# Optimization experiments

Hardware: AMD Instinct MI355X
Metric: run time of the kernel (lower is better)

The kernel has to match this reference:

```python
import jax, jax.numpy as jnp
import numpy as np

N_LETTERS = 256
EMBED_DIM = 1024
HIDDEN_DIM = 2048
SEQ_LEN = 4096


def setup_inputs() -> dict:
    key = jax.random.key(0)
    ks = jax.random.split(key, 8)
    s_e = 1.0 / np.sqrt(EMBED_DIM)
    s_h = 1.0 / np.sqrt(HIDDEN_DIM)
    return {
        "input_ids": jax.random.randint(ks[0], (SEQ_LEN,), 0, N_LETTERS, dtype=jnp.int64)
        if jax.config.jax_enable_x64 else jax.random.randint(ks[0], (SEQ_LEN,), 0, N_LETTERS, dtype=jnp.int32),
        "h0": jnp.zeros((1, 1, HIDDEN_DIM), jnp.float32),
        "c0": jnp.zeros((1, 1, HIDDEN_DIM), jnp.float32),
        "W_emb": jax.random.normal(ks[1], (N_LETTERS, EMBED_DIM), jnp.float32),
        "W_ih": jax.random.normal(ks[2], (4 * HIDDEN_DIM, EMBED_DIM), jnp.float32) * s_e,
        "W_hh": jax.random.normal(ks[3], (4 * HIDDEN_DIM, HIDDEN_DIM), jnp.float32) * s_h,
        "b_ih": jnp.zeros((4 * HIDDEN_DIM,), jnp.float32),
        "b_hh": jnp.zeros((4 * HIDDEN_DIM,), jnp.float32),
        "W_out": jax.random.normal(ks[4], (N_LETTERS, HIDDEN_DIM), jnp.float32) * s_h,
        "b_out": jnp.zeros((N_LETTERS,), jnp.float32),
    }


def reference(input_ids, h0, c0, W_emb, W_ih, W_hh, b_ih, b_hh, W_out, b_out):
    H = W_hh.shape[1]
    emb = W_emb[input_ids]                       # [L, E]
    # Precompute the input-side gate projections for all timesteps (batched GEMM).
    x_gates = emb @ W_ih.T + (b_ih + b_hh)       # [L, 4H]

    def step(carry, xg):
        h, c = carry                             # [H], [H]
        gates = xg + W_hh @ h                    # [4H], PyTorch order i,f,g,o
        i = jax.nn.sigmoid(gates[0 * H:1 * H])
        f = jax.nn.sigmoid(gates[1 * H:2 * H])
        g = jnp.tanh(gates[2 * H:3 * H])
        o = jax.nn.sigmoid(gates[3 * H:4 * H])
        c_new = f * c + i * g
        h_new = o * jnp.tanh(c_new)
        return (h_new, c_new), h_new

    (hL, cL), hs = jax.lax.scan(step, (h0[0, 0], c0[0, 0]), x_gates)  # hs: [L, H]
    logits = hs @ W_out.T + b_out                # [L, n_letters]
    # Dropout(p=0.1) is identity in eval mode.
    out = jax.nn.log_softmax(jax.nn.relu(logits), axis=-1)
    return out, hL[None, None, :], cL[None, None, :]
```

## Files before the change

kernel.cpp:

```cpp
#include <hip/hip_runtime.h>
#include <hip/hip_bf16.h>

#define SEQ 4096
#define EMB 1024
#define HID 2048
#define G4  8192
#define NL  256

typedef __attribute__((ext_vector_type(8))) short bf16x8;
typedef __attribute__((ext_vector_type(4))) float f32x4;

static __device__ __forceinline__ unsigned short f2bf(float f) {
    unsigned int x = __builtin_bit_cast(unsigned int, f);
    return (unsigned short)((x + 0x7FFFu + ((x >> 16) & 1u)) >> 16);
}
static __device__ __forceinline__ float bf2f(unsigned short u) {
    return __builtin_bit_cast(float, ((unsigned int)u) << 16);
}
static __device__ __forceinline__ unsigned long long aload(const unsigned long long* p) {
    return __hip_atomic_load(p, __ATOMIC_RELAXED, __HIP_MEMORY_SCOPE_AGENT);
}
static __device__ __forceinline__ float fsigm(float x) {
    return 1.f / (1.f + __expf(-x));
}
static __device__ __forceinline__ float ftanh(float x) {
    return 1.f - 2.f / (__expf(2.f * x) + 1.f);
}

__global__ __launch_bounds__(256) void k_f2b(const float* __restrict__ in,
                                             unsigned short* __restrict__ out, int n) {
    int i = (blockIdx.x * 256 + threadIdx.x) * 4;
    if (i < n) {
        float4 v = *(const float4*)&in[i];
        ushort4 u;
        u.x = f2bf(v.x); u.y = f2bf(v.y); u.z = f2bf(v.z); u.w = f2bf(v.w);
        *(ushort4*)&out[i] = u;
    }
}

__global__ __launch_bounds__(256) void k_emb(const int* __restrict__ ids,
                                             const float* __restrict__ W_emb,
                                             unsigned short* __restrict__ out) {
    int t = blockIdx.x;
    int e0 = threadIdx.x * 4;
    const float4 v = *(const float4*)&W_emb[(size_t)ids[t] * EMB + e0];
    ushort4 u;
    u.x = f2bf(v.x); u.y = f2bf(v.y); u.z = f2bf(v.z); u.w = f2bf(v.w);
    *(ushort4*)&out[(size_t)t * EMB + e0] = u;
}

#define BM 128
#define BN 128
#define BK 32
__global__ __launch_bounds__(256) void k_gemm_bt(
    const unsigned short* __restrict__ A, const unsigned short* __restrict__ B,
    const float* __restrict__ bias1, const float* __restrict__ bias2,
    float* __restrict__ Cf, unsigned short* __restrict__ Cb,
    int M, int N, int K)
{
    __shared__ unsigned short As[BM * BK];
    __shared__ unsigned short Bs[BN * BK];
    const int bm = blockIdx.x * BM;
    const int bn = blockIdx.y * BN;
    const int tid = threadIdx.x;
    const int wave = tid >> 6, lane = tid & 63;
    const int wm = (wave & 1) * 64, wn = (wave >> 1) * 64;
    const int row16 = lane & 15, quad = lane >> 4;

    f32x4 acc[4][4];
#pragma unroll
    for (int i = 0; i < 4; ++i)
#pragma unroll
        for (int j = 0; j < 4; ++j) acc[i][j] = (f32x4){0.f, 0.f, 0.f, 0.f};

    for (int k0 = 0; k0 < K; k0 += BK) {
        __syncthreads();
#pragma unroll
        for (int s = 0; s < 2; ++s) {
            int c = tid + s * 256;
            int r = c >> 2, col = (c & 3) * 8;
            *(uint4*)&As[r * BK + col] = *(const uint4*)&A[(size_t)(bm + r) * K + k0 + col];
            *(uint4*)&Bs[r * BK + col] = *(const uint4*)&B[(size_t)(bn + r) * K + k0 + col];
        }
        __syncthreads();
        bf16x8 af[4], bfr[4];
#pragma unroll
        for (int i = 0; i < 4; ++i) {
            af[i]  = *(const bf16x8*)&As[(wm + i * 16 + row16) * BK + quad * 8];
            bfr[i] = *(const bf16x8*)&Bs[(wn + i * 16 + row16) * BK + quad * 8];
        }
#pragma unroll
        for (int i = 0; i < 4; ++i)
#pragma unroll
            for (int j = 0; j < 4; ++j)
                acc[i][j] = __builtin_amdgcn_mfma_f32_16x16x32_bf16(af[i], bfr[j], acc[i][j], 0, 0, 0);
    }

#pragma unroll
    for (int j = 0; j < 4; ++j) {
        int col = bn + wn + j * 16 + row16;
        float bsum = (bias1 ? bias1[col] : 0.f) + (bias2 ? bias2[col] : 0.f);
#pragma unroll
        for (int i = 0; i < 4; ++i) {
#pragma unroll
            for (int r = 0; r < 4; ++r) {
                int row = bm + wm + i * 16 + quad * 4 + r;
                float v = acc[i][j][r] + bsum;
                if (Cf) Cf[(size_t)row * N + col] = v;
                else    Cb[(size_t)row * N + col] = f2bf(v);
            }
        }
    }
}

#define LSTM_LDS 90112
__global__ __launch_bounds__(1024, 1) void k_lstm(
    const unsigned short* __restrict__ Whhb,
    const unsigned short* __restrict__ xg,
    const float* __restrict__ h0, const float* __restrict__ c0,
    unsigned short* __restrict__ hsb,
    float* __restrict__ outHC,
    unsigned long long* __restrict__ hcomm)
{
    extern __shared__ char smem[];
    float* LDSp = (float*)smem;

    const int b = blockIdx.x, tid = threadIdx.x;
    const int wave = tid >> 6, lane = tid & 63;
    const int sub = lane & 15, quad = lane >> 4;

    const int qa = (sub >> 3), qb = 2 + (sub >> 3), j = sub & 7;
    const unsigned short* wa = Whhb + ((size_t)(qa * HID + b * 8 + j)) * HID + wave * 128 + quad * 8;
    const unsigned short* wb = Whhb + ((size_t)(qb * HID + b * 8 + j)) * HID + wave * 128 + quad * 8;
    bf16x8 afrA[4], afrB[4];
#pragma unroll
    for (int c = 0; c < 4; ++c) {
        afrA[c] = *(const bf16x8*)(wa + c * 32);
        afrB[c] = *(const bf16x8*)(wb + c * 32);
    }

    float creg = 0.f;
    if (tid < 8) creg = c0[b * 8 + tid];

    for (int t = 0; t < SEQ; ++t) {
        float xq0 = 0.f, xq1 = 0.f, xq2 = 0.f, xq3 = 0.f;
        if (wave == 0 && lane < 8) {
            const unsigned short* xr = xg + (size_t)t * G4 + b * 8 + lane;
            xq0 = bf2f(xr[0]);
            xq1 = bf2f(xr[2048]);
            xq2 = bf2f(xr[4096]);
            xq3 = bf2f(xr[6144]);
        }

        f32x4 acc0 = (f32x4){0.f, 0.f, 0.f, 0.f};
        f32x4 acc1 = (f32x4){0.f, 0.f, 0.f, 0.f};

        if (t == 0) {
#pragma unroll
            for (int c = 0; c < 4; ++c) {
                const float* hp = h0 + wave * 128 + c * 32 + quad * 8;
                float4 va = *(const float4*)hp;
                float4 vb = *(const float4*)(hp + 4);
                uint4 d;
                d.x = (unsigned)f2bf(va.x) | ((unsigned)f2bf(va.y) << 16);
                d.y = (unsigned)f2bf(va.z) | ((unsigned)f2bf(va.w) << 16);
                d.z = (unsigned)f2bf(vb.x) | ((unsigned)f2bf(vb.y) << 16);
                d.w = (unsigned)f2bf(vb.z) | ((unsigned)f2bf(vb.w) << 16);
                bf16x8 hf = __builtin_bit_cast(bf16x8, d);
                acc0 = __builtin_amdgcn_mfma_f32_16x16x32_bf16(afrA[c], hf, acc0, 0, 0, 0);
                acc1 = __builtin_amdgcn_mfma_f32_16x16x32_bf16(afrB[c], hf, acc1, 0, 0, 0);
            }
        } else {
            const unsigned long long* src =
                hcomm + (size_t)((t - 1) & 1) * 8192 + (size_t)(b & 7) * 1024 + wave * 64;
            const unsigned tag = (unsigned)t;
            unsigned long long x;
            for (;;) {
                x = aload(&src[lane]);
                if ((unsigned)(x >> 32) == tag) break;
                __builtin_amdgcn_s_sleep(1);
            }
            int myd = (int)(unsigned)x;
#pragma unroll
            for (int c = 0; c < 4; ++c) {
                const int sl = c * 16 + quad * 4;
                uint4 d;
                d.x = (unsigned)__shfl(myd, sl + 0);
                d.y = (unsigned)__shfl(myd, sl + 1);
                d.z = (unsigned)__shfl(myd, sl + 2);
                d.w = (unsigned)__shfl(myd, sl + 3);
                bf16x8 hf = __builtin_bit_cast(bf16x8, d);
                acc0 = __builtin_amdgcn_mfma_f32_16x16x32_bf16(afrA[c], hf, acc0, 0, 0, 0);
                acc1 = __builtin_amdgcn_mfma_f32_16x16x32_bf16(afrB[c], hf, acc1, 0, 0, 0);
            }
        }

        float* P = LDSp + (t & 1) * 640;
        if (sub == 0) {
#pragma unroll
            for (int r = 0; r < 4; ++r) {
                P[(quad * 4 + r) * 20 + wave]      = acc0[r];
                P[(16 + quad * 4 + r) * 20 + wave] = acc1[r];
            }
        }
        __syncthreads();

        if (wave == 0) {
            float g = 0.f;
            if (lane < 32) {
                const float* rp = P + lane * 20;
                f32x4 s = *(const f32x4*)rp;
                s += *(const f32x4*)(rp + 4);
                s += *(const f32x4*)(rp + 8);
                s += *(const f32x4*)(rp + 12);
                g = s[0] + s[1] + s[2] + s[3];
            }
            float gF = __shfl(g, 8 + lane);
            float gG = __shfl(g, 16 + lane);
            float gO = __shfl(g, 24 + lane);
            unsigned hv = 0;
            float cn = 0.f, hn = 0.f;
            if (lane < 8) {
                float gi = g  + xq0;
                float gf = gF + xq1;
                float gg = gG + xq2;
                float go = gO + xq3;
                float i_ = fsigm(gi);
                float f_ = fsigm(gf);
                float g_ = ftanh(gg);
                float o_ = fsigm(go);
                cn = f_ * creg + i_ * g_;
                hn = o_ * ftanh(cn);
                creg = cn;
                hv = (unsigned)f2bf(hn);
            }
            {
                int jj = lane & 3;
                unsigned lo = (unsigned)__shfl((int)hv, 2 * jj);
                unsigned hi = (unsigned)__shfl((int)hv, 2 * jj + 1);
                if (lane < 32) {
                    unsigned long long wrd =
                        (((unsigned long long)(unsigned)(t + 1)) << 32)
                        | (unsigned long long)(lo | (hi << 16));
                    __hip_atomic_store(
                        &hcomm[(size_t)(t & 1) * 8192 + (size_t)(lane >> 2) * 1024 + b * 4 + jj],
                        wrd, __ATOMIC_RELAXED, __HIP_MEMORY_SCOPE_AGENT);
                }
            }
            if (lane < 8) {
                hsb[(size_t)t * HID + b * 8 + lane] = (unsigned short)hv;
                if (t == SEQ - 1) {
                    outHC[b * 8 + lane] = hn;
                    outHC[HID + b * 8 + lane] = cn;
                }
            }
        }
    }
}

__global__ __launch_bounds__(256) void k_softmax(const float* __restrict__ logits,
                                                 float* __restrict__ out) {
    int row = blockIdx.x * 4 + (threadIdx.x >> 6);
    int lane = threadIdx.x & 63;
    const float* Lr = logits + (size_t)row * NL;
    float4 v = *(const float4*)&Lr[lane * 4];
    v.x = fmaxf(v.x, 0.f); v.y = fmaxf(v.y, 0.f);
    v.z = fmaxf(v.z, 0.f); v.w = fmaxf(v.w, 0.f);
    float m = fmaxf(fmaxf(v.x, v.y), fmaxf(v.z, v.w));
#pragma unroll
    for (int off = 32; off > 0; off >>= 1) m = fmaxf(m, __shfl_xor(m, off));
    float e = __expf(v.x - m) + __expf(v.y - m) + __expf(v.z - m) + __expf(v.w - m);
#pragma unroll
    for (int off = 32; off > 0; off >>= 1) e += __shfl_xor(e, off);
    float ls = __logf(e) + m;
    float4 o;
    o.x = v.x - ls; o.y = v.y - ls; o.z = v.z - ls; o.w = v.w - ls;
    *(float4*)&out[(size_t)row * NL + lane * 4] = o;
}

extern "C" void kernel_launch(void* const* d_in, const int* in_sizes, int n_in,
                              void* d_out, int out_size, void* d_ws, size_t ws_size,
                              hipStream_t stream) {
    const int*   ids   = (const int*)d_in[0];
    const float* h0    = (const float*)d_in[1];
    const float* c0    = (const float*)d_in[2];
    const float* W_emb = (const float*)d_in[3];
    const float* W_ih  = (const float*)d_in[4];
    const float* W_hh  = (const float*)d_in[5];
    const float* b_ih  = (const float*)d_in[6];
    const float* b_hh  = (const float*)d_in[7];
    const float* W_out = (const float*)d_in[8];
    const float* b_out = (const float*)d_in[9];
    float* out = (float*)d_out;

    char* ws = (char*)d_ws;
    unsigned short* xg    = (unsigned short*)(ws);
    unsigned short* hsb   = (unsigned short*)(ws + 67108864);
    unsigned short* Wihb  = (unsigned short*)(ws + 83886080);
    unsigned short* embb  = (unsigned short*)(ws + 100663296);
    unsigned short* Woutb = (unsigned short*)(ws + 109051904);
    float*          logit = (float*)(ws + 110100480);
    unsigned short* Whhb  = (unsigned short*)(ws + 114294784);
    unsigned long long* hcomm = (unsigned long long*)(ws + 147849216);

    k_f2b<<<(G4 * EMB / 4 + 255) / 256, 256, 0, stream>>>(W_ih, Wihb, G4 * EMB);
    k_f2b<<<(NL * HID / 4 + 255) / 256, 256, 0, stream>>>(W_out, Woutb, NL * HID);
    k_f2b<<<(G4 * HID / 4 + 255) / 256, 256, 0, stream>>>(W_hh, Whhb, G4 * HID);
    k_emb<<<SEQ, 256, 0, stream>>>(ids, W_emb, embb);

    dim3 g1(SEQ / BM, G4 / BN);
    k_gemm_bt<<<g1, 256, 0, stream>>>(embb, Wihb, b_ih, b_hh, nullptr, xg, SEQ, G4, EMB);

    hipFuncSetAttribute((const void*)k_lstm, hipFuncAttributeMaxDynamicSharedMemorySize, LSTM_LDS);
    k_lstm<<<256, 1024, LSTM_LDS, stream>>>(Whhb, xg, h0, c0, hsb, out + (size_t)SEQ * NL, hcomm);

    dim3 g2(SEQ / BM, NL / BN);
    k_gemm_bt<<<g2, 256, 0, stream>>>(hsb, Woutb, b_out, nullptr, logit, nullptr, SEQ, NL, HID);

    k_softmax<<<SEQ / 4, 256, 0, stream>>>(logit, out);
}
```

Baseline: 10.61 ms.

## Interleave x_gates layout, split MFMA chains, tune polling and prioritize gate wave

The GEMM that produces bf16 x_gates now writes them gate-interleaved, so each hidden unit's four gate values sit next to each other. The LSTM step can then fetch them with one 8-byte load instead of four strided loads. The MFMA accumulation is split into two independent chains per gate half to shorten the dependency chain. Polling for the previous hidden state first checks immediately, then sleeps longer between retries to reduce memory traffic. The wave on the critical gate-compute and broadcast path is given raised scheduling priority.

```diff
diff --git a/kernel.cpp b/kernel.cpp
--- a/kernel.cpp
+++ b/kernel.cpp
@@ -107,7 +107,7 @@
                 int row = bm + wm + i * 16 + quad * 4 + r;
                 float v = acc[i][j][r] + bsum;
                 if (Cf) Cf[(size_t)row * N + col] = v;
-                else    Cb[(size_t)row * N + col] = f2bf(v);
+                else    Cb[(size_t)row * N + ((col & 2047) << 2) + (col >> 11)] = f2bf(v);
             }
         }
     }
@@ -145,15 +145,17 @@
     for (int t = 0; t < SEQ; ++t) {
         float xq0 = 0.f, xq1 = 0.f, xq2 = 0.f, xq3 = 0.f;
         if (wave == 0 && lane < 8) {
-            const unsigned short* xr = xg + (size_t)t * G4 + b * 8 + lane;
-            xq0 = bf2f(xr[0]);
-            xq1 = bf2f(xr[2048]);
-            xq2 = bf2f(xr[4096]);
-            xq3 = bf2f(xr[6144]);
-        }
-
-        f32x4 acc0 = (f32x4){0.f, 0.f, 0.f, 0.f};
-        f32x4 acc1 = (f32x4){0.f, 0.f, 0.f, 0.f};
+            uint2 w2 = *(const uint2*)(xg + (size_t)t * G4 + (size_t)(b * 8 + lane) * 4);
+            xq0 = bf2f((unsigned short)(w2.x & 0xffff));
+            xq1 = bf2f((unsigned short)(w2.x >> 16));
+            xq2 = bf2f((unsigned short)(w2.y & 0xffff));
+            xq3 = bf2f((unsigned short)(w2.y >> 16));
+        }
+
+        f32x4 accA0 = (f32x4){0.f, 0.f, 0.f, 0.f};
+        f32x4 accA1 = (f32x4){0.f, 0.f, 0.f, 0.f};
+        f32x4 accB0 = (f32x4){0.f, 0.f, 0.f, 0.f};
+        f32x4 accB1 = (f32x4){0.f, 0.f, 0.f, 0.f};
 
         if (t == 0) {
 #pragma unroll
@@ -167,18 +169,26 @@
                 d.z = (unsigned)f2bf(vb.x) | ((unsigned)f2bf(vb.y) << 16);
                 d.w = (unsigned)f2bf(vb.z) | ((unsigned)f2bf(vb.w) << 16);
                 bf16x8 hf = __builtin_bit_cast(bf16x8, d);
-                acc0 = __builtin_amdgcn_mfma_f32_16x16x32_bf16(afrA[c], hf, acc0, 0, 0, 0);
-                acc1 = __builtin_amdgcn_mfma_f32_16x16x32_bf16(afrB[c], hf, acc1, 0, 0, 0);
+                if (c < 2) {
+                    accA0 = __builtin_amdgcn_mfma_f32_16x16x32_bf16(afrA[c], hf, accA0, 0, 0, 0);
+                    accB0 = __builtin_amdgcn_mfma_f32_16x16x32_bf16(afrB[c], hf, accB0, 0, 0, 0);
+                } else {
+                    accA1 = __builtin_amdgcn_mfma_f32_16x16x32_bf16(afrA[c], hf, accA1, 0, 0, 0);
+                    accB1 = __builtin_amdgcn_mfma_f32_16x16x32_bf16(afrB[c], hf, accB1, 0, 0, 0);
+                }
             }
         } else {
             const unsigned long long* src =
                 hcomm + (size_t)((t - 1) & 1) * 8192 + (size_t)(b & 7) * 1024 + wave * 64;
             const unsigned tag = (unsigned)t;
-            unsigned long long x;
-            for (;;) {
-                x = aload(&src[lane]);
-                if ((unsigned)(x >> 32) == tag) break;
-                __builtin_amdgcn_s_sleep(1);
+            unsigned long long x = aload(&src[lane]);
+            if ((unsigned)(x >> 32) != tag) {
+                __builtin_amdgcn_s_sleep(8);
+                for (;;) {
+                    x = aload(&src[lane]);
+                    if ((unsigned)(x >> 32) == tag) break;
+                    __builtin_amdgcn_s_sleep(2);
+                }
             }
             int myd = (int)(unsigned)x;
 #pragma unroll
@@ -190,10 +200,17 @@
                 d.z = (unsigned)__shfl(myd, sl + 2);
                 d.w = (unsigned)__shfl(myd, sl + 3);
                 bf16x8 hf = __builtin_bit_cast(bf16x8, d);
-                acc0 = __builtin_amdgcn_mfma_f32_16x16x32_bf16(afrA[c], hf, acc0, 0, 0, 0);
-                acc1 = __builtin_amdgcn_mfma_f32_16x16x32_bf16(afrB[c], hf, acc1, 0, 0, 0);
-            }
-        }
+                if (c < 2) {
+                    accA0 = __builtin_amdgcn_mfma_f32_16x16x32_bf16(afrA[c], hf, accA0, 0, 0, 0);
+                    accB0 = __builtin_amdgcn_mfma_f32_16x16x32_bf16(afrB[c], hf, accB0, 0, 0, 0);
+                } else {
+                    accA1 = __builtin_amdgcn_mfma_f32_16x16x32_bf16(afrA[c], hf, accA1, 0, 0, 0);
+                    accB1 = __builtin_amdgcn_mfma_f32_16x16x32_bf16(afrB[c], hf, accB1, 0, 0, 0);
+                }
+            }
+        }
+        f32x4 acc0 = accA0 + accA1;
+        f32x4 acc1 = accB0 + accB1;
 
         float* P = LDSp + (t & 1) * 640;
         if (sub == 0) {
@@ -206,6 +223,7 @@
         __syncthreads();
 
         if (wave == 0) {
+            __builtin_amdgcn_s_setprio(1);
             float g = 0.f;
             if (lane < 32) {
                 const float* rp = P + lane * 20;
@@ -247,6 +265,7 @@
                         wrd, __ATOMIC_RELAXED, __HIP_MEMORY_SCOPE_AGENT);
                 }
             }
+            __builtin_amdgcn_s_setprio(0);
             if (lane < 8) {
                 hsb[(size_t)t * HID + b * 8 + lane] = (unsigned short)hv;
                 if (t == SEQ - 1) {
```

Result: faster. 10.31 ms (-2.8%).

## Halve LSTM persistent blocks, 16 units per block with interleaved gate layout

Applied to the files above, without the earlier changes.

Each persistent LSTM block now owns 16 hidden units instead of 8, so 128 blocks run instead of 256. Each wave issues four MFMAs per k-chunk covering all four gates. The input-gate GEMM output is stored gate-interleaved, so each unit's four gate preactivations load as one 8-byte read. The change also swaps the sigmoid/tanh divisions for hardware reciprocals, polls twice per spin iteration after an initial sleep, and raises wave-0 priority during the gate update. The aim is to cut the number of blocks taking part in each step's cross-block handshake and the latency of the per-step critical path, at the cost of more work per block per step.

```diff
diff --git a/kernel.cpp b/kernel.cpp
--- a/kernel.cpp
+++ b/kernel.cpp
@@ -20,11 +20,14 @@
 static __device__ __forceinline__ unsigned long long aload(const unsigned long long* p) {
     return __hip_atomic_load(p, __ATOMIC_RELAXED, __HIP_MEMORY_SCOPE_AGENT);
 }
+static __device__ __forceinline__ float frcp(float x) {
+    return __builtin_amdgcn_rcpf(x);
+}
 static __device__ __forceinline__ float fsigm(float x) {
-    return 1.f / (1.f + __expf(-x));
+    return frcp(1.f + __expf(-x));
 }
 static __device__ __forceinline__ float ftanh(float x) {
-    return 1.f - 2.f / (__expf(2.f * x) + 1.f);
+    return 1.f - 2.f * frcp(__expf(2.f * x) + 1.f);
 }
 
 __global__ __launch_bounds__(256) void k_f2b(const float* __restrict__ in,
@@ -107,12 +110,14 @@
                 int row = bm + wm + i * 16 + quad * 4 + r;
                 float v = acc[i][j][r] + bsum;
                 if (Cf) Cf[(size_t)row * N + col] = v;
-                else    Cb[(size_t)row * N + col] = f2bf(v);
-            }
-        }
-    }
-}
-
+                else    Cb[(size_t)row * N + ((col & 2047) << 2) + (col >> 11)] = f2bf(v);
+            }
+        }
+    }
+}
+
+#define NBLK 128
+#define UPB  16
 #define LSTM_LDS 90112
 __global__ __launch_bounds__(1024, 1) void k_lstm(
     const unsigned short* __restrict__ Whhb,
@@ -129,36 +134,36 @@
     const int wave = tid >> 6, lane = tid & 63;
     const int sub = lane & 15, quad = lane >> 4;
 
-    const int qa = (sub >> 3), qb = 2 + (sub >> 3), j = sub & 7;
-    const unsigned short* wa = Whhb + ((size_t)(qa * HID + b * 8 + j)) * HID + wave * 128 + quad * 8;
-    const unsigned short* wb = Whhb + ((size_t)(qb * HID + b * 8 + j)) * HID + wave * 128 + quad * 8;
-    bf16x8 afrA[4], afrB[4];
-#pragma unroll
-    for (int c = 0; c < 4; ++c) {
-        afrA[c] = *(const bf16x8*)(wa + c * 32);
-        afrB[c] = *(const bf16x8*)(wb + c * 32);
+    bf16x8 afr[4][4];
+#pragma unroll
+    for (int q = 0; q < 4; ++q) {
+        const unsigned short* wp =
+            Whhb + ((size_t)(q * HID + b * UPB + sub)) * HID + wave * 128 + quad * 8;
+#pragma unroll
+        for (int kc = 0; kc < 4; ++kc) afr[q][kc] = *(const bf16x8*)(wp + kc * 32);
     }
 
     float creg = 0.f;
-    if (tid < 8) creg = c0[b * 8 + tid];
+    if (tid < UPB) creg = c0[b * UPB + tid];
 
     for (int t = 0; t < SEQ; ++t) {
         float xq0 = 0.f, xq1 = 0.f, xq2 = 0.f, xq3 = 0.f;
-        if (wave == 0 && lane < 8) {
-            const unsigned short* xr = xg + (size_t)t * G4 + b * 8 + lane;
-            xq0 = bf2f(xr[0]);
-            xq1 = bf2f(xr[2048]);
-            xq2 = bf2f(xr[4096]);
-            xq3 = bf2f(xr[6144]);
-        }
-
-        f32x4 acc0 = (f32x4){0.f, 0.f, 0.f, 0.f};
-        f32x4 acc1 = (f32x4){0.f, 0.f, 0.f, 0.f};
+        if (wave == 0 && lane < UPB) {
+            uint2 w2 = *(const uint2*)(xg + (size_t)t * G4 + (size_t)(b * UPB + lane) * 4);
+            xq0 = bf2f((unsigned short)(w2.x & 0xffff));
+            xq1 = bf2f((unsigned short)(w2.x >> 16));
+            xq2 = bf2f((unsigned short)(w2.y & 0xffff));
+            xq3 = bf2f((unsigned short)(w2.y >> 16));
+        }
+
+        f32x4 acc[4];
+#pragma unroll
+        for (int q = 0; q < 4; ++q) acc[q] = (f32x4){0.f, 0.f, 0.f, 0.f};
 
         if (t == 0) {
 #pragma unroll
-            for (int c = 0; c < 4; ++c) {
-                const float* hp = h0 + wave * 128 + c * 32 + quad * 8;
+            for (int kc = 0; kc < 4; ++kc) {
+                const float* hp = h0 + wave * 128 + kc * 32 + quad * 8;
                 float4 va = *(const float4*)hp;
                 float4 vb = *(const float4*)(hp + 4);
                 uint4 d;
@@ -167,91 +172,91 @@
                 d.z = (unsigned)f2bf(vb.x) | ((unsigned)f2bf(vb.y) << 16);
                 d.w = (unsigned)f2bf(vb.z) | ((unsigned)f2bf(vb.w) << 16);
                 bf16x8 hf = __builtin_bit_cast(bf16x8, d);
-                acc0 = __builtin_amdgcn_mfma_f32_16x16x32_bf16(afrA[c], hf, acc0, 0, 0, 0);
-                acc1 = __builtin_amdgcn_mfma_f32_16x16x32_bf16(afrB[c], hf, acc1, 0, 0, 0);
+#pragma unroll
+                for (int q = 0; q < 4; ++q)
+                    acc[q] = __builtin_amdgcn_mfma_f32_16x16x32_bf16(afr[q][kc], hf, acc[q], 0, 0, 0);
             }
         } else {
             const unsigned long long* src =
                 hcomm + (size_t)((t - 1) & 1) * 8192 + (size_t)(b & 7) * 1024 + wave * 64;
             const unsigned tag = (unsigned)t;
-            unsigned long long x;
-            for (;;) {
-                x = aload(&src[lane]);
-                if ((unsigned)(x >> 32) == tag) break;
-                __builtin_amdgcn_s_sleep(1);
+            unsigned long long x = aload(&src[lane]);
+            if ((unsigned)(x >> 32) != tag) {
+                __builtin_amdgcn_s_sleep(8);
+                for (;;) {
+                    unsigned long long x1 = aload(&src[lane]);
+                    unsigned long long x2 = aload(&src[lane]);
+                    if ((unsigned)(x1 >> 32) == tag) { x = x1; break; }
+                    if ((unsigned)(x2 >> 32) == tag) { x = x2; break; }
+                    __builtin_amdgcn_s_sleep(1);
+                }
             }
             int myd = (int)(unsigned)x;
 #pragma unroll
-            for (int c = 0; c < 4; ++c) {
-                const int sl = c * 16 + quad * 4;
+            for (int kc = 0; kc < 4; ++kc) {
+                const int sl = kc * 16 + quad * 4;
                 uint4 d;
                 d.x = (unsigned)__shfl(myd, sl + 0);
                 d.y = (unsigned)__shfl(myd, sl + 1);
                 d.z = (unsigned)__shfl(myd, sl + 2);
                 d.w = (unsigned)__shfl(myd, sl + 3);
                 bf16x8 hf = __builtin_bit_cast(bf16x8, d);
-                acc0 = __builtin_amdgcn_mfma_f32_16x16x32_bf16(afrA[c], hf, acc0, 0, 0, 0);
-                acc1 = __builtin_amdgcn_mfma_f32_16x16x32_bf16(afrB[c], hf, acc1, 0, 0, 0);
-            }
-        }
-
-        float* P = LDSp + (t & 1) * 640;
+#pragma unroll
+                for (int q = 0; q < 4; ++q)
+                    acc[q] = __builtin_amdgcn_mfma_f32_16x16x32_bf16(afr[q][kc], hf, acc[q], 0, 0, 0);
+            }
+        }
+
+        float* P = LDSp + (t & 1) * 1280;
         if (sub == 0) {
 #pragma unroll
-            for (int r = 0; r < 4; ++r) {
-                P[(quad * 4 + r) * 20 + wave]      = acc0[r];
-                P[(16 + quad * 4 + r) * 20 + wave] = acc1[r];
-            }
+            for (int q = 0; q < 4; ++q)
+#pragma unroll
+                for (int r = 0; r < 4; ++r)
+                    P[(q * 16 + quad * 4 + r) * 20 + wave] = acc[q][r];
         }
         __syncthreads();
 
         if (wave == 0) {
-            float g = 0.f;
-            if (lane < 32) {
-                const float* rp = P + lane * 20;
-                f32x4 s = *(const f32x4*)rp;
-                s += *(const f32x4*)(rp + 4);
-                s += *(const f32x4*)(rp + 8);
-                s += *(const f32x4*)(rp + 12);
-                g = s[0] + s[1] + s[2] + s[3];
-            }
-            float gF = __shfl(g, 8 + lane);
-            float gG = __shfl(g, 16 + lane);
-            float gO = __shfl(g, 24 + lane);
+            __builtin_amdgcn_s_setprio(1);
+            const float* rp = P + lane * 20;
+            f32x4 s = *(const f32x4*)rp;
+            s += *(const f32x4*)(rp + 4);
+            s += *(const f32x4*)(rp + 8);
+            s += *(const f32x4*)(rp + 12);
+            float g = s[0] + s[1] + s[2] + s[3];
+            float gF = __shfl(g, 16 + (lane & 15));
+            float gG = __shfl(g, 32 + (lane & 15));
+            float gO = __shfl(g, 48 + (lane & 15));
             unsigned hv = 0;
             float cn = 0.f, hn = 0.f;
-            if (lane < 8) {
-                float gi = g  + xq0;
-                float gf = gF + xq1;
-                float gg = gG + xq2;
-                float go = gO + xq3;
-                float i_ = fsigm(gi);
-                float f_ = fsigm(gf);
-                float g_ = ftanh(gg);
-                float o_ = fsigm(go);
+            if (lane < UPB) {
+                float i_ = fsigm(g + xq0);
+                float f_ = fsigm(gF + xq1);
+                float g_ = ftanh(gG + xq2);
+                float o_ = fsigm(gO + xq3);
                 cn = f_ * creg + i_ * g_;
                 hn = o_ * ftanh(cn);
                 creg = cn;
                 hv = (unsigned)f2bf(hn);
             }
             {
-                int jj = lane & 3;
+                int jj = lane & 7;
                 unsigned lo = (unsigned)__shfl((int)hv, 2 * jj);
                 unsigned hi = (unsigned)__shfl((int)hv, 2 * jj + 1);
-                if (lane < 32) {
-                    unsigned long long wrd =
-                        (((unsigned long long)(unsigned)(t + 1)) << 32)
-                        | (unsigned long long)(lo | (hi << 16));
-                    __hip_atomic_store(
-                        &hcomm[(size_t)(t & 1) * 8192 + (size_t)(lane >> 2) * 1024 + b * 4 + jj],
-                        wrd, __ATOMIC_RELAXED, __HIP_MEMORY_SCOPE_AGENT);
-                }
-            }
-            if (lane < 8) {
-                hsb[(size_t)t * HID + b * 8 + lane] = (unsigned short)hv;
+                unsigned long long wrd =
+                    (((unsigned long long)(unsigned)(t + 1)) << 32)
+                    | (unsigned long long)(lo | (hi << 16));
+                (void)__hip_atomic_exchange(
+                    &hcomm[(size_t)(t & 1) * 8192 + (size_t)(lane >> 3) * 1024 + b * 8 + jj],
+                    wrd, __ATOMIC_RELAXED, __HIP_MEMORY_SCOPE_AGENT);
+            }
+            __builtin_amdgcn_s_setprio(0);
+            if (lane < UPB) {
+                hsb[(size_t)t * HID + b * UPB + lane] = (unsigned short)hv;
                 if (t == SEQ - 1) {
-                    outHC[b * 8 + lane] = hn;
-                    outHC[HID + b * 8 + lane] = cn;
+                    outHC[b * UPB + lane] = hn;
+                    outHC[HID + b * UPB + lane] = cn;
                 }
             }
         }
@@ -312,7 +317,7 @@
     k_gemm_bt<<<g1, 256, 0, stream>>>(embb, Wihb, b_ih, b_hh, nullptr, xg, SEQ, G4, EMB);
 
     hipFuncSetAttribute((const void*)k_lstm, hipFuncAttributeMaxDynamicSharedMemorySize, LSTM_LDS);
-    k_lstm<<<256, 1024, LSTM_LDS, stream>>>(Whhb, xg, h0, c0, hsb, out + (size_t)SEQ * NL, hcomm);
+    k_lstm<<<NBLK, 1024, LSTM_LDS, stream>>>(Whhb, xg, h0, c0, hsb, out + (size_t)SEQ * NL, hcomm);
 
     dim3 g2(SEQ / BM, NL / BN);
     k_gemm_bt<<<g2, 256, 0, stream>>>(hsb, Woutb, b_out, nullptr, logit, nullptr, SEQ, NL, HID);
```

New measurement: 10.66 ms. No clear change (+0.5%).
